# Kernel tuning notes

Measured on AMD Instinct MI355X. Metric: run time of the kernel, lower is better.

## Reference

```python
import jax, jax.numpy as jnp
import numpy as np

N = 100000   # nodes
E = 1600000  # edges
F = 128      # node_feature_dim
H = 128      # hidden_dim
O = 256      # output_dim
G = 256      # number of graphs in the batch


def setup_inputs() -> dict:
    key = jax.random.key(0)
    ks = jax.random.split(key, 12)
    x = jax.random.normal(ks[0], (N, F), dtype=jnp.float32)
    edge_index = jax.random.randint(ks[1], (2, E), 0, N, dtype=jnp.int64)
    batch = jnp.sort(jax.random.randint(ks[2], (N,), 0, G, dtype=jnp.int64))

    def lin(k, fan_in, shape):
        return (jax.random.normal(k, shape, dtype=jnp.float32) / np.float32(np.sqrt(fan_in)))

    W1 = lin(ks[3], F, (F, H)); b1 = jnp.zeros((H,), jnp.float32)
    W2 = lin(ks[4], H, (H, H)); b2 = jnp.zeros((H,), jnp.float32)
    W3 = lin(ks[5], H, (H, H)); b3 = jnp.zeros((H,), jnp.float32)
    Wfc = lin(ks[6], H, (H, O))
    bfc = lin(ks[7], H, (O,))
    return {"x": x, "W1": W1, "b1": b1, "W2": W2, "b2": b2,
            "W3": W3, "b3": b3, "Wfc": Wfc, "bfc": bfc,
            "edge_index": edge_index, "batch": batch}


def _gcn_norm(edge_index, n_nodes):
    # PyG GCNConv default: add self-loops, symmetric normalization.
    loop = jnp.arange(n_nodes, dtype=edge_index.dtype)
    row = jnp.concatenate([edge_index[0], loop])  # source
    col = jnp.concatenate([edge_index[1], loop])  # target
    deg = jax.ops.segment_sum(jnp.ones_like(col, dtype=jnp.float32), col,
                              num_segments=n_nodes)
    dinv = jnp.where(deg > 0, jax.lax.rsqrt(deg), 0.0)
    norm = dinv[row] * dinv[col]  # [E+N]
    return row, col, norm


def _gcn_conv(x, W, b, row, col, norm, n_nodes):
    h = x @ W                                   # transform first (PyG order)
    msg = norm[:, None] * h[row]                # gather + scale
    out = jax.ops.segment_sum(msg, col, num_segments=n_nodes)  # scatter-add
    return out + b


def reference(x, W1, b1, W2, b2, W3, b3, Wfc, bfc, edge_index, batch):
    n_nodes = x.shape[0]
    row, col, norm = _gcn_norm(edge_index, n_nodes)
    h = jax.nn.relu(_gcn_conv(x, W1, b1, row, col, norm, n_nodes))
    h = jax.nn.relu(_gcn_conv(h, W2, b2, row, col, norm, n_nodes))
    h = jax.nn.relu(_gcn_conv(h, W3, b3, row, col, norm, n_nodes))
    # global_mean_pool over graph ids
    sums = jax.ops.segment_sum(h, batch, num_segments=G)
    cnt = jax.ops.segment_sum(jnp.ones((n_nodes,), jnp.float32), batch,
                              num_segments=G)
    pooled = sums / jnp.maximum(cnt, 1.0)[:, None]
    return pooled @ Wfc + bfc
```

## Files before the change

kernel.cpp:

```cpp
#include <hip/hip_runtime.h>

#define NF 128
#define NH 128
#define NO 256
#define NG 256

typedef unsigned int   u32;
typedef unsigned short u16;
typedef __attribute__((ext_vector_type(8))) short short8;
typedef __attribute__((ext_vector_type(4))) float floatx4;

__device__ __forceinline__ float bflo(u32 g) { return __uint_as_float(g << 16); }
__device__ __forceinline__ float bfhi(u32 g) { return __uint_as_float(g & 0xffff0000u); }
__device__ __forceinline__ u16 f2bf(float x) {
    u32 u = __float_as_uint(x);
    u += 0x7fffu + ((u >> 16) & 1u);
    return (u16)(u >> 16);
}
__device__ __forceinline__ u32 packbf2(float x, float y) {
    u32 ux = __float_as_uint(x); ux += 0x7fffu + ((ux >> 16) & 1u);
    u32 uy = __float_as_uint(y); uy += 0x7fffu + ((uy >> 16) & 1u);
    return (ux >> 16) | (uy & 0xffff0000u);
}


__global__ __launch_bounds__(256) void setup_kernel(const float* __restrict__ W1,
                                                    const float* __restrict__ W2,
                                                    const float* __restrict__ W3,
                                                    u16* __restrict__ Wt1, u16* __restrict__ Wt2,
                                                    u16* __restrict__ Wt3,
                                                    const int* __restrict__ col, int E,
                                                    int* __restrict__ bucketCnt) {
    int b = blockIdx.x;
    int t = threadIdx.x;
    if (b < 192) {
        int idx = b * 256 + t;
        int w = idx >> 14;
        int r = idx & 16383;
        const float* W = (w == 0) ? W1 : (w == 1) ? W2 : W3;
        u16* Wt = (w == 0) ? Wt1 : (w == 1) ? Wt2 : Wt3;
        int k = r >> 7, c = r & 127;
        Wt[c * NF + k] = f2bf(W[r]);
        return;
    }
    __shared__ int h[256];
    h[t] = 0;
    __syncthreads();
    int base = (b - 192) * 4096;
    #pragma unroll
    for (int i = 0; i < 16; ++i) {
        int e = base + i * 256 + t;
        if (e < E) atomicAdd(&h[col[e] >> 9], 1);
    }
    __syncthreads();
    if (h[t]) atomicAdd(&bucketCnt[t], h[t]);
}

__global__ void scan_buckets(const int* __restrict__ bucketCnt, int* __restrict__ cbase,
                             int* __restrict__ gcur, float* __restrict__ pooled) {
    __shared__ int sh[256];
    int t = threadIdx.x;
    int v = bucketCnt[t];
    sh[t] = v; __syncthreads();
    for (int d = 1; d < 256; d <<= 1) {
        int x = (t >= d) ? sh[t - d] : 0;
        __syncthreads();
        sh[t] += x;
        __syncthreads();
    }
    cbase[t] = sh[t] - v;
    gcur[t]  = sh[t] - v;
    float4 z = make_float4(0.f, 0.f, 0.f, 0.f);
    float4* p4 = (float4*)pooled;
    #pragma unroll
    for (int i = 0; i < 32; ++i) p4[i * 256 + t] = z;
}


__global__ __launch_bounds__(256) void bin_coarse(const int* __restrict__ row,
                                                  const int* __restrict__ col,
                                                  int* __restrict__ gcur,
                                                  u32* __restrict__ coarse, int E) {
    __shared__ u32 cnt[256];
    __shared__ u32 lcur[256];
    __shared__ u32 gbase[256];
    __shared__ u32 sc[256];
    __shared__ u32 packed[4096];
    int t = threadIdx.x;
    int base = blockIdx.x * 4096;
    cnt[t] = 0;
    __syncthreads();

    u32 rv[16], cv[16];
    #pragma unroll
    for (int i = 0; i < 16; ++i) {
        int e = base + i * 256 + t;
        if (e < E) {
            rv[i] = (u32)row[e];
            cv[i] = (u32)col[e];
            atomicAdd(&cnt[cv[i] >> 9], 1u);
        }
    }
    __syncthreads();
    u32 own = cnt[t];
    sc[t] = own; __syncthreads();
    for (int d = 1; d < 256; d <<= 1) {
        u32 x = (t >= d) ? sc[t - d] : 0;
        __syncthreads();
        sc[t] += x;
        __syncthreads();
    }
    u32 excl = sc[t] - own;
    u32 total = sc[255];
    if (own > 0) gbase[t] = (u32)atomicAdd(&gcur[t], (int)own);
    cnt[t]  = excl;
    lcur[t] = excl;
    __syncthreads();

    #pragma unroll
    for (int i = 0; i < 16; ++i) {
        int e = base + i * 256 + t;
        if (e < E) {
            u32 p = atomicAdd(&lcur[cv[i] >> 9], 1u);
            packed[p] = rv[i] | ((cv[i] & 511u) << 17);
        }
    }
    __syncthreads();

    for (u32 i = t; i < total; i += 256) {
        u32 lo = 0, hi = 255;
        while (lo < hi) { u32 mid = (lo + hi + 1) >> 1; if (cnt[mid] <= i) lo = mid; else hi = mid - 1; }
        coarse[gbase[lo] + (i - cnt[lo])] = packed[i];
    }
}


__global__ __launch_bounds__(256) void build_csr_bucket(const u32* __restrict__ coarse,
                                                        const int* __restrict__ cbase,
                                                        const int* __restrict__ bucketCnt,
                                                        u32* __restrict__ srcs,
                                                        int* __restrict__ deg,
                                                        float* __restrict__ dinv,
                                                        int* __restrict__ offs, int N) {
    __shared__ u32 buf[10240];
    __shared__ u32 hist[512];
    __shared__ u32 scn[512];
    __shared__ u32 tmp[512];
    __shared__ u32 cur[512];
    int t = threadIdx.x;
    int b = blockIdx.x;
    int lo = b << 9;
    if (lo >= N) return;
    int cnt  = bucketCnt[b];
    int base = cbase[b];

    for (int j = t; j < 512; j += 256) hist[j] = 0;
    __syncthreads();
    for (int i = t; i < cnt; i += 256) {
        u32 pk = coarse[base + i];
        buf[i] = pk;
        atomicAdd(&hist[pk >> 17], 1u);
    }
    __syncthreads();
    for (int j = t; j < 512; j += 256) scn[j] = hist[j];
    __syncthreads();
    for (int d = 1; d < 512; d <<= 1) {
        for (int j = t; j < 512; j += 256) tmp[j] = (j >= d) ? scn[j - d] : 0u;
        __syncthreads();
        for (int j = t; j < 512; j += 256) scn[j] += tmp[j];
        __syncthreads();
    }
    int hi = min(lo + 512, N) - lo;
    for (int j = t; j < 512; j += 256) {
        u32 excl = scn[j] - hist[j];
        cur[j] = excl;
        if (j < hi) {
            deg[lo + j]  = (int)hist[j];
            dinv[lo + j] = rsqrtf((float)hist[j] + 1.0f);
            offs[lo + j] = base + (int)excl;
        }
    }
    __syncthreads();
    for (int i = t; i < cnt; i += 256) {
        u32 pk = buf[i];
        u32 c = pk >> 17;
        u32 p = atomicAdd(&cur[c], 1u);
        srcs[base + p] = pk & 0x1ffffu;
    }
}


__device__ __forceinline__ void gemm_tile(u16* As, const u16* Wt, const float* dinv,
                                          u16* C, int n, int node0, int t) {
    int wv = t >> 6;
    int l  = t & 63;
    int lr = l & 15;
    int lq = l >> 4;

    floatx4 acc[8];
    #pragma unroll
    for (int c = 0; c < 8; ++c) acc[c] = (floatx4){0.f, 0.f, 0.f, 0.f};

    #pragma unroll
    for (int kk = 0; kk < 4; ++kk) {
        short8 af = *(const short8*)&As[(wv * 16 + lr) * 136 + kk * 32 + lq * 8];
        #pragma unroll
        for (int c = 0; c < 8; ++c) {
            short8 bf = *(const short8*)&Wt[(c * 16 + lr) * 136 + kk * 32 + lq * 8];
            acc[c] = __builtin_amdgcn_mfma_f32_16x16x32_bf16(af, bf, acc[c], 0, 0, 0);
        }
    }

    float* Cs = (float*)As;
    #pragma unroll
    for (int h = 0; h < 2; ++h) {
        __syncthreads();
        if ((wv >> 1) == h) {
            int lrow = (wv & 1) * 16 + lq * 4;
            #pragma unroll
            for (int c = 0; c < 8; ++c)
                #pragma unroll
                for (int r = 0; r < 4; ++r)
                    Cs[(lrow + r) * 132 + c * 16 + lr] = acc[c][r];
        }
        __syncthreads();
        int nd = t >> 3, seg = t & 7;
        int node = node0 + h * 32 + nd;
        if (node < n) {
            float di = dinv[node];
            const float* src = &Cs[nd * 132 + seg * 16];
            u32 o[8];
            #pragma unroll
            for (int i = 0; i < 8; ++i) o[i] = packbf2(di * src[2 * i], di * src[2 * i + 1]);
            uint4* dst = (uint4*)(C + (size_t)node * NH + seg * 16);
            dst[0] = make_uint4(o[0], o[1], o[2], o[3]);
            dst[1] = make_uint4(o[4], o[5], o[6], o[7]);
        }
    }
    __syncthreads();
}

__global__ __launch_bounds__(256) void gemm_mfma(const u16* __restrict__ A,
                                                 const u16* __restrict__ Wtg,
                                                 const float* __restrict__ dinv,
                                                 u16* __restrict__ C, int n, int ntiles) {
    __shared__ u16 Wt[128 * 136];
    __shared__ u16 As[64 * 136];
    int t = threadIdx.x;

    const uint4* Wg = (const uint4*)Wtg;
    #pragma unroll
    for (int i = 0; i < 8; ++i) {
        int idx = t + 256 * i;
        int cc = idx >> 4, q = idx & 15;
        *(uint4*)&Wt[cc * 136 + q * 8] = Wg[cc * 16 + q];
    }

    for (int tile = blockIdx.x; tile < ntiles; tile += gridDim.x) {
        int node0 = tile * 64;
        const uint4* Ag = (const uint4*)A;
        #pragma unroll
        for (int i = 0; i < 4; ++i) {
            int idx = t + 256 * i;
            int nd = idx >> 4, q = idx & 15;
            uint4 v = make_uint4(0, 0, 0, 0);
            if (node0 + nd < n) v = Ag[(size_t)(node0 + nd) * 16 + q];
            *(uint4*)&As[nd * 136 + q * 8] = v;
        }
        __syncthreads();
        gemm_tile(As, Wt, dinv, C, n, node0, t);
    }
}

__global__ __launch_bounds__(256) void gemm_mfma_f32(const float* __restrict__ A,
                                                     const u16* __restrict__ Wtg,
                                                     const float* __restrict__ dinv,
                                                     u16* __restrict__ C, int n, int ntiles) {
    __shared__ u16 Wt[128 * 136];
    __shared__ u16 As[64 * 136];
    int t = threadIdx.x;

    const uint4* Wg = (const uint4*)Wtg;
    #pragma unroll
    for (int i = 0; i < 8; ++i) {
        int idx = t + 256 * i;
        int cc = idx >> 4, q = idx & 15;
        *(uint4*)&Wt[cc * 136 + q * 8] = Wg[cc * 16 + q];
    }

    for (int tile = blockIdx.x; tile < ntiles; tile += gridDim.x) {
        int node0 = tile * 64;
        const float4* Ag = (const float4*)A;
        #pragma unroll
        for (int i = 0; i < 8; ++i) {
            int idx = t + 256 * i;
            int nd = idx >> 5, q = idx & 31;
            float4 v = make_float4(0.f, 0.f, 0.f, 0.f);
            if (node0 + nd < n) v = Ag[(size_t)(node0 + nd) * 32 + q];
            uint2 p; p.x = packbf2(v.x, v.y); p.y = packbf2(v.z, v.w);
            *(uint2*)&As[nd * 136 + q * 4] = p;
        }
        __syncthreads();
        gemm_tile(As, Wt, dinv, C, n, node0, t);
    }
}


__global__ __launch_bounds__(256) void gcn_aggregate(const u16* __restrict__ gtab,
                                                     const u32* __restrict__ srcs,
                                                     const int* __restrict__ offs,
                                                     const int* __restrict__ deg,
                                                     const float* __restrict__ dinv,
                                                     const float* __restrict__ bias,
                                                     u16* __restrict__ outb, int n) {
    int wv = threadIdx.x >> 6;
    int l  = threadIdx.x & 63;
    int node = blockIdx.x * 4 + wv;
    if (node >= n) return;
    int start = offs[node];
    int end   = start + deg[node];
    const u32* rows = (const u32*)gtab;

    float a0 = 0.f, a1 = 0.f;
    int k = start;
    for (; k + 16 <= end; k += 16) {
        u32 gv[16];
        #pragma unroll
        for (int i = 0; i < 16; ++i) {
            u32 s = srcs[k + i];
            gv[i] = rows[(size_t)s * 64 + l];
        }
        #pragma unroll
        for (int i = 0; i < 16; ++i) { a0 += bflo(gv[i]); a1 += bfhi(gv[i]); }
    }
    for (; k + 4 <= end; k += 4) {
        u32 s0 = srcs[k], s1 = srcs[k + 1], s2 = srcs[k + 2], s3 = srcs[k + 3];
        u32 g0 = rows[(size_t)s0 * 64 + l];
        u32 g1 = rows[(size_t)s1 * 64 + l];
        u32 g2 = rows[(size_t)s2 * 64 + l];
        u32 g3 = rows[(size_t)s3 * 64 + l];
        a0 += bflo(g0) + bflo(g1) + bflo(g2) + bflo(g3);
        a1 += bfhi(g0) + bfhi(g1) + bfhi(g2) + bfhi(g3);
    }
    for (; k < end; ++k) {
        u32 g = rows[(size_t)srcs[k] * 64 + l];
        a0 += bflo(g); a1 += bfhi(g);
    }
    u32 gs = rows[(size_t)node * 64 + l];
    a0 += bflo(gs); a1 += bfhi(gs);
    float di = dinv[node];
    float2 bb = *(const float2*)&bias[l * 2];
    a0 = fmaxf(di * a0 + bb.x, 0.f);
    a1 = fmaxf(di * a1 + bb.y, 0.f);
    ((u32*)outb)[(size_t)node * 64 + l] = packbf2(a0, a1);
}


__global__ __launch_bounds__(256) void pool_partial(const u16* __restrict__ h,
                                                    const int* __restrict__ batch,
                                                    float* __restrict__ pooled, int n) {
    int t = threadIdx.x;
    int j = t & 127, half = t >> 7;
    int bs = blockIdx.x * 128;
    int be = min(bs + 128, n);
    float acc = 0.f;
    int cur = -1;
    for (int i = bs + half; i < be; i += 2) {
        int g = batch[i];
        if (g != cur) {
            if (cur >= 0) atomicAdd(&pooled[(size_t)cur * NH + j], acc);
            acc = 0.f; cur = g;
        }
        acc += __uint_as_float((u32)h[(size_t)i * NH + j] << 16);
    }
    if (cur >= 0) atomicAdd(&pooled[(size_t)cur * NH + j], acc);
}


__global__ __launch_bounds__(256) void final_fc(const float* __restrict__ pooled,
                                                const int* __restrict__ batch,
                                                const float* __restrict__ Wfc,
                                                const float* __restrict__ bfc,
                                                float* __restrict__ out, int n) {
    int g = blockIdx.x;
    int tid = threadIdx.x;

    int lo = 0, hi = n;
    while (lo < hi) { int m = (lo + hi) >> 1; if (batch[m] < g) lo = m + 1; else hi = m; }
    int start = lo;
    hi = n;
    while (lo < hi) { int m = (lo + hi) >> 1; if (batch[m] < g + 1) lo = m + 1; else hi = m; }
    int end = lo;

    __shared__ float pr[NH];
    float inv = 1.0f / fmaxf((float)(end - start), 1.0f);
    if (tid < NH) pr[tid] = pooled[(size_t)g * NH + tid] * inv;
    __syncthreads();

    float o = bfc[tid];
    #pragma unroll 8
    for (int k = 0; k < NH; ++k) o += pr[k] * Wfc[(size_t)k * NO + tid];
    out[(size_t)g * NO + tid] = o;
}


extern "C" void kernel_launch(void* const* d_in, const int* in_sizes, int n_in,
                              void* d_out, int out_size, void* d_ws, size_t ws_size,
                              hipStream_t stream) {
    const float* x   = (const float*)d_in[0];
    const float* W1  = (const float*)d_in[1];
    const float* b1  = (const float*)d_in[2];
    const float* W2  = (const float*)d_in[3];
    const float* b2  = (const float*)d_in[4];
    const float* W3  = (const float*)d_in[5];
    const float* b3  = (const float*)d_in[6];
    const float* Wfc = (const float*)d_in[7];
    const float* bfc = (const float*)d_in[8];
    const int*   ei  = (const int*)d_in[9];
    const int*   bat = (const int*)d_in[10];
    float* out = (float*)d_out;

    const int N = in_sizes[0] / NF;
    const int E = in_sizes[9] / 2;
    const int* rowp = ei;
    const int* colp = ei + E;

    char* w = (char*)d_ws;
    u32* srcs    = (u32*)w;                      w += (size_t)E * 4;
    u32* coarse  = (u32*)w;                      w += (size_t)E * 4;
    u16* hA   = (u16*)w;                         w += (size_t)N * NH * 2;
    u16* hB   = (u16*)w;                         w += (size_t)N * NH * 2;
    u16* tmpb = (u16*)w;                         w += (size_t)N * NH * 2;
    u16* Wt1  = (u16*)w;                         w += NF * NH * 2;
    u16* Wt2  = (u16*)w;                         w += NF * NH * 2;
    u16* Wt3  = (u16*)w;                         w += NF * NH * 2;
    float* dinv = (float*)w;                     w += (size_t)N * 4;
    int* degc   = (int*)w;                       w += (size_t)N * 4;
    int* offs   = (int*)w;                       w += (size_t)N * 4;
    float* pooled = (float*)w;                   w += (size_t)NG * NH * 4;
    int* bucketCnt = (int*)w;                    w += 256 * 4;
    int* cbase  = (int*)w;                       w += 256 * 4;
    int* gcur   = (int*)w;                       w += 256 * 4;

    const int TB = 256;
    int ntiles = (N + 63) / 64;
    int gGemmP = (ntiles < 768) ? ntiles : 768;
    int gAgg  = (N + 3) / 4;
    int gPool = (N + 127) / 128;
    int NB = (N + 511) >> 9;
    int gBin = (E + 4095) / 4096;

    hipMemsetAsync(bucketCnt, 0, 256 * 4, stream);

    setup_kernel<<<192 + gBin, TB, 0, stream>>>(W1, W2, W3, Wt1, Wt2, Wt3, colp, E, bucketCnt);
    scan_buckets<<<1, 256, 0, stream>>>(bucketCnt, cbase, gcur, pooled);
    bin_coarse<<<gBin, TB, 0, stream>>>(rowp, colp, gcur, coarse, E);
    build_csr_bucket<<<NB, TB, 0, stream>>>(coarse, cbase, bucketCnt, srcs, degc, dinv, offs, N);

    gemm_mfma_f32<<<gGemmP, TB, 0, stream>>>(x, Wt1, dinv, tmpb, N, ntiles);
    gcn_aggregate<<<gAgg, TB, 0, stream>>>(tmpb, srcs, offs, degc, dinv, b1, hB, N);

    gemm_mfma<<<gGemmP, TB, 0, stream>>>(hB, Wt2, dinv, tmpb, N, ntiles);
    gcn_aggregate<<<gAgg, TB, 0, stream>>>(tmpb, srcs, offs, degc, dinv, b2, hA, N);

    gemm_mfma<<<gGemmP, TB, 0, stream>>>(hA, Wt3, dinv, tmpb, N, ntiles);
    gcn_aggregate<<<gAgg, TB, 0, stream>>>(tmpb, srcs, offs, degc, dinv, b3, hB, N);

    pool_partial<<<gPool, TB, 0, stream>>>(hB, bat, pooled, N);
    final_fc<<<NG, NO, 0, stream>>>(pooled, bat, Wfc, bfc, out, N);
}
```

Measured before the change: 455.1 us.

## Use finer CSR buckets, prefetch GEMM tiles, widen pooling, batch final FC

Bucket count for CSR construction doubles to 512 buckets of 256 nodes, so build_csr_bucket runs more, smaller blocks with less shared memory and a simpler scan; overflow beyond the buffer falls back to global reads. Both GEMM kernels register-prefetch the next tile's activations while computing the current tile, hiding global load latency. Pooling reads packed bf16 pairs with four rows per pass, and final_fc handles eight graphs per block to reuse Wfc loads. More register pressure in GEMM and more atomics in binning are the tradeoffs.

```diff
diff --git a/kernel.cpp b/kernel.cpp
--- a/kernel.cpp
+++ b/kernel.cpp
@@ -43,26 +43,27 @@
         Wt[c * NF + k] = f2bf(W[r]);
         return;
     }
-    __shared__ int h[256];
-    h[t] = 0;
+    __shared__ int h[512];
+    h[t] = 0; h[t + 256] = 0;
     __syncthreads();
     int base = (b - 192) * 4096;
     #pragma unroll
     for (int i = 0; i < 16; ++i) {
         int e = base + i * 256 + t;
-        if (e < E) atomicAdd(&h[col[e] >> 9], 1);
-    }
-    __syncthreads();
-    if (h[t]) atomicAdd(&bucketCnt[t], h[t]);
+        if (e < E) atomicAdd(&h[col[e] >> 8], 1);
+    }
+    __syncthreads();
+    if (h[t])       atomicAdd(&bucketCnt[t], h[t]);
+    if (h[t + 256]) atomicAdd(&bucketCnt[t + 256], h[t + 256]);
 }
 
 __global__ void scan_buckets(const int* __restrict__ bucketCnt, int* __restrict__ cbase,
                              int* __restrict__ gcur, float* __restrict__ pooled) {
-    __shared__ int sh[256];
+    __shared__ int sh[512];
     int t = threadIdx.x;
     int v = bucketCnt[t];
     sh[t] = v; __syncthreads();
-    for (int d = 1; d < 256; d <<= 1) {
+    for (int d = 1; d < 512; d <<= 1) {
         int x = (t >= d) ? sh[t - d] : 0;
         __syncthreads();
         sh[t] += x;
@@ -73,7 +74,7 @@
     float4 z = make_float4(0.f, 0.f, 0.f, 0.f);
     float4* p4 = (float4*)pooled;
     #pragma unroll
-    for (int i = 0; i < 32; ++i) p4[i * 256 + t] = z;
+    for (int i = 0; i < 16; ++i) p4[i * 512 + t] = z;
 }
 
 
@@ -81,14 +82,15 @@
                                                   const int* __restrict__ col,
                                                   int* __restrict__ gcur,
                                                   u32* __restrict__ coarse, int E) {
-    __shared__ u32 cnt[256];
-    __shared__ u32 lcur[256];
-    __shared__ u32 gbase[256];
-    __shared__ u32 sc[256];
+    __shared__ u32 cnt[512];
+    __shared__ u32 lcur[512];
+    __shared__ u32 gbase[512];
+    __shared__ u32 sc[512];
+    __shared__ u32 tmp[512];
     __shared__ u32 packed[4096];
     int t = threadIdx.x;
     int base = blockIdx.x * 4096;
-    cnt[t] = 0;
+    cnt[t] = 0; cnt[t + 256] = 0;
     __syncthreads();
 
     u32 rv[16], cv[16];
@@ -98,39 +100,42 @@
         if (e < E) {
             rv[i] = (u32)row[e];
             cv[i] = (u32)col[e];
-            atomicAdd(&cnt[cv[i] >> 9], 1u);
-        }
-    }
-    __syncthreads();
-    u32 own = cnt[t];
-    sc[t] = own; __syncthreads();
-    for (int d = 1; d < 256; d <<= 1) {
-        u32 x = (t >= d) ? sc[t - d] : 0;
-        __syncthreads();
-        sc[t] += x;
-        __syncthreads();
-    }
-    u32 excl = sc[t] - own;
-    u32 total = sc[255];
-    if (own > 0) gbase[t] = (u32)atomicAdd(&gcur[t], (int)own);
-    cnt[t]  = excl;
-    lcur[t] = excl;
+            atomicAdd(&cnt[cv[i] >> 8], 1u);
+        }
+    }
+    __syncthreads();
+    for (int j = t; j < 512; j += 256) sc[j] = cnt[j];
+    __syncthreads();
+    for (int d = 1; d < 512; d <<= 1) {
+        for (int j = t; j < 512; j += 256) tmp[j] = (j >= d) ? sc[j - d] : 0u;
+        __syncthreads();
+        for (int j = t; j < 512; j += 256) sc[j] += tmp[j];
+        __syncthreads();
+    }
+    u32 total = sc[511];
+    for (int j = t; j < 512; j += 256) {
+        u32 own = cnt[j];
+        u32 excl = sc[j] - own;
+        if (own > 0) gbase[j] = (u32)atomicAdd(&gcur[j], (int)own);
+        lcur[j] = excl;
+        tmp[j]  = excl;
+    }
     __syncthreads();
 
     #pragma unroll
     for (int i = 0; i < 16; ++i) {
         int e = base + i * 256 + t;
         if (e < E) {
-            u32 p = atomicAdd(&lcur[cv[i] >> 9], 1u);
-            packed[p] = rv[i] | ((cv[i] & 511u) << 17);
+            u32 p = atomicAdd(&lcur[cv[i] >> 8], 1u);
+            packed[p] = rv[i] | ((cv[i] & 255u) << 17);
         }
     }
     __syncthreads();
 
     for (u32 i = t; i < total; i += 256) {
-        u32 lo = 0, hi = 255;
-        while (lo < hi) { u32 mid = (lo + hi + 1) >> 1; if (cnt[mid] <= i) lo = mid; else hi = mid - 1; }
-        coarse[gbase[lo] + (i - cnt[lo])] = packed[i];
+        u32 lo = 0, hi = 511;
+        while (lo < hi) { u32 mid = (lo + hi + 1) >> 1; if (tmp[mid] <= i) lo = mid; else hi = mid - 1; }
+        coarse[gbase[lo] + (i - tmp[lo])] = packed[i];
     }
 }
 
@@ -142,47 +147,44 @@
                                                         int* __restrict__ deg,
                                                         float* __restrict__ dinv,
                                                         int* __restrict__ offs, int N) {
-    __shared__ u32 buf[10240];
-    __shared__ u32 hist[512];
-    __shared__ u32 scn[512];
-    __shared__ u32 tmp[512];
-    __shared__ u32 cur[512];
+    __shared__ u32 buf[6144];
+    __shared__ u32 hist[256];
+    __shared__ u32 scn[256];
+    __shared__ u32 cur[256];
     int t = threadIdx.x;
     int b = blockIdx.x;
-    int lo = b << 9;
+    int lo = b << 8;
     if (lo >= N) return;
     int cnt  = bucketCnt[b];
     int base = cbase[b];
 
-    for (int j = t; j < 512; j += 256) hist[j] = 0;
+    hist[t] = 0;
     __syncthreads();
     for (int i = t; i < cnt; i += 256) {
         u32 pk = coarse[base + i];
-        buf[i] = pk;
+        if (i < 6144) buf[i] = pk;
         atomicAdd(&hist[pk >> 17], 1u);
     }
     __syncthreads();
-    for (int j = t; j < 512; j += 256) scn[j] = hist[j];
-    __syncthreads();
-    for (int d = 1; d < 512; d <<= 1) {
-        for (int j = t; j < 512; j += 256) tmp[j] = (j >= d) ? scn[j - d] : 0u;
-        __syncthreads();
-        for (int j = t; j < 512; j += 256) scn[j] += tmp[j];
-        __syncthreads();
-    }
-    int hi = min(lo + 512, N) - lo;
-    for (int j = t; j < 512; j += 256) {
-        u32 excl = scn[j] - hist[j];
-        cur[j] = excl;
-        if (j < hi) {
-            deg[lo + j]  = (int)hist[j];
-            dinv[lo + j] = rsqrtf((float)hist[j] + 1.0f);
-            offs[lo + j] = base + (int)excl;
-        }
+    scn[t] = hist[t];
+    __syncthreads();
+    for (int d = 1; d < 256; d <<= 1) {
+        u32 x = (t >= d) ? scn[t - d] : 0u;
+        __syncthreads();
+        scn[t] += x;
+        __syncthreads();
+    }
+    u32 excl = scn[t] - hist[t];
+    cur[t] = excl;
+    int node = lo + t;
+    if (node < N) {
+        deg[node]  = (int)hist[t];
+        dinv[node] = rsqrtf((float)hist[t] + 1.0f);
+        offs[node] = base + (int)excl;
     }
     __syncthreads();
     for (int i = t; i < cnt; i += 256) {
-        u32 pk = buf[i];
+        u32 pk = (i < 6144) ? buf[i] : coarse[base + i];
         u32 c = pk >> 17;
         u32 p = atomicAdd(&cur[c], 1u);
         srcs[base + p] = pk & 0x1ffffu;
@@ -256,19 +258,39 @@
         *(uint4*)&Wt[cc * 136 + q * 8] = Wg[cc * 16 + q];
     }
 
-    for (int tile = blockIdx.x; tile < ntiles; tile += gridDim.x) {
+    const uint4* Ag = (const uint4*)A;
+    uint4 pv[4];
+    int tile = blockIdx.x;
+    if (tile < ntiles) {
         int node0 = tile * 64;
-        const uint4* Ag = (const uint4*)A;
         #pragma unroll
         for (int i = 0; i < 4; ++i) {
             int idx = t + 256 * i;
             int nd = idx >> 4, q = idx & 15;
-            uint4 v = make_uint4(0, 0, 0, 0);
-            if (node0 + nd < n) v = Ag[(size_t)(node0 + nd) * 16 + q];
-            *(uint4*)&As[nd * 136 + q * 8] = v;
-        }
-        __syncthreads();
-        gemm_tile(As, Wt, dinv, C, n, node0, t);
+            pv[i] = make_uint4(0, 0, 0, 0);
+            if (node0 + nd < n) pv[i] = Ag[(size_t)(node0 + nd) * 16 + q];
+        }
+    }
+    for (; tile < ntiles; tile += gridDim.x) {
+        #pragma unroll
+        for (int i = 0; i < 4; ++i) {
+            int idx = t + 256 * i;
+            int nd = idx >> 4, q = idx & 15;
+            *(uint4*)&As[nd * 136 + q * 8] = pv[i];
+        }
+        __syncthreads();
+        int nxt = tile + gridDim.x;
+        if (nxt < ntiles) {
+            int node0n = nxt * 64;
+            #pragma unroll
+            for (int i = 0; i < 4; ++i) {
+                int idx = t + 256 * i;
+                int nd = idx >> 4, q = idx & 15;
+                pv[i] = make_uint4(0, 0, 0, 0);
+                if (node0n + nd < n) pv[i] = Ag[(size_t)(node0n + nd) * 16 + q];
+            }
+        }
+        gemm_tile(As, Wt, dinv, C, n, tile * 64, t);
     }
 }
 
@@ -288,20 +310,40 @@
         *(uint4*)&Wt[cc * 136 + q * 8] = Wg[cc * 16 + q];
     }
 
-    for (int tile = blockIdx.x; tile < ntiles; tile += gridDim.x) {
+    const float4* Ag = (const float4*)A;
+    float4 pv[8];
+    int tile = blockIdx.x;
+    if (tile < ntiles) {
         int node0 = tile * 64;
-        const float4* Ag = (const float4*)A;
         #pragma unroll
         for (int i = 0; i < 8; ++i) {
             int idx = t + 256 * i;
             int nd = idx >> 5, q = idx & 31;
-            float4 v = make_float4(0.f, 0.f, 0.f, 0.f);
-            if (node0 + nd < n) v = Ag[(size_t)(node0 + nd) * 32 + q];
-            uint2 p; p.x = packbf2(v.x, v.y); p.y = packbf2(v.z, v.w);
+            pv[i] = make_float4(0.f, 0.f, 0.f, 0.f);
+            if (node0 + nd < n) pv[i] = Ag[(size_t)(node0 + nd) * 32 + q];
+        }
+    }
+    for (; tile < ntiles; tile += gridDim.x) {
+        #pragma unroll
+        for (int i = 0; i < 8; ++i) {
+            int idx = t + 256 * i;
+            int nd = idx >> 5, q = idx & 31;
+            uint2 p; p.x = packbf2(pv[i].x, pv[i].y); p.y = packbf2(pv[i].z, pv[i].w);
             *(uint2*)&As[nd * 136 + q * 4] = p;
         }
         __syncthreads();
-        gemm_tile(As, Wt, dinv, C, n, node0, t);
+        int nxt = tile + gridDim.x;
+        if (nxt < ntiles) {
+            int node0n = nxt * 64;
+            #pragma unroll
+            for (int i = 0; i < 8; ++i) {
+                int idx = t + 256 * i;
+                int nd = idx >> 5, q = idx & 31;
+                pv[i] = make_float4(0.f, 0.f, 0.f, 0.f);
+                if (node0n + nd < n) pv[i] = Ag[(size_t)(node0n + nd) * 32 + q];
+            }
+        }
+        gemm_tile(As, Wt, dinv, C, n, tile * 64, t);
     }
 }
 
@@ -360,20 +402,28 @@
                                                     const int* __restrict__ batch,
                                                     float* __restrict__ pooled, int n) {
     int t = threadIdx.x;
-    int j = t & 127, half = t >> 7;
+    int ju = t & 63, sub = t >> 6;
     int bs = blockIdx.x * 128;
     int be = min(bs + 128, n);
-    float acc = 0.f;
+    const u32* h32 = (const u32*)h;
+    float a0 = 0.f, a1 = 0.f;
     int cur = -1;
-    for (int i = bs + half; i < be; i += 2) {
+    for (int i = bs + sub; i < be; i += 4) {
         int g = batch[i];
         if (g != cur) {
-            if (cur >= 0) atomicAdd(&pooled[(size_t)cur * NH + j], acc);
-            acc = 0.f; cur = g;
-        }
-        acc += __uint_as_float((u32)h[(size_t)i * NH + j] << 16);
-    }
-    if (cur >= 0) atomicAdd(&pooled[(size_t)cur * NH + j], acc);
+            if (cur >= 0) {
+                atomicAdd(&pooled[(size_t)cur * NH + 2 * ju], a0);
+                atomicAdd(&pooled[(size_t)cur * NH + 2 * ju + 1], a1);
+            }
+            a0 = 0.f; a1 = 0.f; cur = g;
+        }
+        u32 v = h32[(size_t)i * 64 + ju];
+        a0 += bflo(v); a1 += bfhi(v);
+    }
+    if (cur >= 0) {
+        atomicAdd(&pooled[(size_t)cur * NH + 2 * ju], a0);
+        atomicAdd(&pooled[(size_t)cur * NH + 2 * ju + 1], a1);
+    }
 }
 
 
@@ -382,25 +432,39 @@
                                                 const float* __restrict__ Wfc,
                                                 const float* __restrict__ bfc,
                                                 float* __restrict__ out, int n) {
-    int g = blockIdx.x;
+    int g0 = blockIdx.x * 8;
     int tid = threadIdx.x;
-
-    int lo = 0, hi = n;
-    while (lo < hi) { int m = (lo + hi) >> 1; if (batch[m] < g) lo = m + 1; else hi = m; }
-    int start = lo;
-    hi = n;
-    while (lo < hi) { int m = (lo + hi) >> 1; if (batch[m] < g + 1) lo = m + 1; else hi = m; }
-    int end = lo;
-
-    __shared__ float pr[NH];
-    float inv = 1.0f / fmaxf((float)(end - start), 1.0f);
-    if (tid < NH) pr[tid] = pooled[(size_t)g * NH + tid] * inv;
-    __syncthreads();
-
-    float o = bfc[tid];
-    #pragma unroll 8
-    for (int k = 0; k < NH; ++k) o += pr[k] * Wfc[(size_t)k * NO + tid];
-    out[(size_t)g * NO + tid] = o;
+    __shared__ float pr[8][NH];
+    __shared__ float invc[8];
+
+    if (tid < 8) {
+        int g = g0 + tid;
+        int lo = 0, hi = n;
+        while (lo < hi) { int m = (lo + hi) >> 1; if (batch[m] < g) lo = m + 1; else hi = m; }
+        int start = lo;
+        hi = n;
+        while (lo < hi) { int m = (lo + hi) >> 1; if (batch[m] < g + 1) lo = m + 1; else hi = m; }
+        invc[tid] = 1.0f / fmaxf((float)(lo - start), 1.0f);
+    }
+    __syncthreads();
+    for (int i = tid; i < 8 * NH; i += 256) {
+        int gi = i >> 7, j = i & 127;
+        pr[gi][j] = pooled[(size_t)(g0 + gi) * NH + j] * invc[gi];
+    }
+    __syncthreads();
+
+    float bv = bfc[tid];
+    float acc[8];
+    #pragma unroll
+    for (int gi = 0; gi < 8; ++gi) acc[gi] = bv;
+    for (int k = 0; k < NH; ++k) {
+        float w = Wfc[(size_t)k * NO + tid];
+        #pragma unroll
+        for (int gi = 0; gi < 8; ++gi) acc[gi] += pr[gi][k] * w;
+    }
+    #pragma unroll
+    for (int gi = 0; gi < 8; ++gi)
+        out[(size_t)(g0 + gi) * NO + tid] = acc[gi];
 }
 
 
@@ -438,22 +502,22 @@
     int* degc   = (int*)w;                       w += (size_t)N * 4;
     int* offs   = (int*)w;                       w += (size_t)N * 4;
     float* pooled = (float*)w;                   w += (size_t)NG * NH * 4;
-    int* bucketCnt = (int*)w;                    w += 256 * 4;
-    int* cbase  = (int*)w;                       w += 256 * 4;
-    int* gcur   = (int*)w;                       w += 256 * 4;
+    int* bucketCnt = (int*)w;                    w += 512 * 4;
+    int* cbase  = (int*)w;                       w += 512 * 4;
+    int* gcur   = (int*)w;                       w += 512 * 4;
 
     const int TB = 256;
     int ntiles = (N + 63) / 64;
     int gGemmP = (ntiles < 768) ? ntiles : 768;
     int gAgg  = (N + 3) / 4;
     int gPool = (N + 127) / 128;
-    int NB = (N + 511) >> 9;
+    int NB = (N + 255) >> 8;
     int gBin = (E + 4095) / 4096;
 
-    hipMemsetAsync(bucketCnt, 0, 256 * 4, stream);
+    hipMemsetAsync(bucketCnt, 0, 512 * 4, stream);
 
     setup_kernel<<<192 + gBin, TB, 0, stream>>>(W1, W2, W3, Wt1, Wt2, Wt3, colp, E, bucketCnt);
-    scan_buckets<<<1, 256, 0, stream>>>(bucketCnt, cbase, gcur, pooled);
+    scan_buckets<<<1, 512, 0, stream>>>(bucketCnt, cbase, gcur, pooled);
     bin_coarse<<<gBin, TB, 0, stream>>>(rowp, colp, gcur, coarse, E);
     build_csr_bucket<<<NB, TB, 0, stream>>>(coarse, cbase, bucketCnt, srcs, degc, dinv, offs, N);
 
@@ -467,5 +531,5 @@
     gcn_aggregate<<<gAgg, TB, 0, stream>>>(tmpb, srcs, offs, degc, dinv, b3, hB, N);
 
     pool_partial<<<gPool, TB, 0, stream>>>(hB, bat, pooled, N);
-    final_fc<<<NG, NO, 0, stream>>>(pooled, bat, Wfc, bfc, out, N);
-}
+    final_fc<<<NG / 8, NO, 0, stream>>>(pooled, bat, Wfc, bfc, out, N);
+}
```

New measurement: 432.2 us, median of 2. 5.0% less time.
